# Kernel tuning notes

Measured on AMD Instinct MI355X. Metric: run time of the kernel, lower is better.

Reference implementation:

```python
import jax, jax.numpy as jnp
import numpy as np

B, L, DIM = 2, 2048, 1024
N_HEADS = 16
HEAD = DIM // N_HEADS  # 64


def setup_inputs() -> dict:
    key = jax.random.key(0)
    ks = jax.random.split(key, 7)
    s = 1.0 / np.sqrt(DIM)
    return {
        "q": jax.random.normal(ks[0], (B, L, DIM), jnp.float32),
        "k": jax.random.normal(ks[1], (B, L, DIM), jnp.float32),
        "v": jax.random.normal(ks[2], (B, L, DIM), jnp.float32),
        "Wq": jax.random.normal(ks[3], (DIM, DIM), jnp.float32) * s,
        "Wk": jax.random.normal(ks[4], (DIM, DIM), jnp.float32) * s,
        "Wv": jax.random.normal(ks[5], (DIM, DIM), jnp.float32) * s,
        "Wo": jax.random.normal(ks[6], (DIM, DIM), jnp.float32) * s,
    }


def reference(q, k, v, Wq, Wk, Wv, Wo):
    b, l, dim = q.shape
    # nn.Linear(bias=False): x @ W.T
    qp = (q @ Wq.T).reshape(b, N_HEADS, l, HEAD)  # faithful: plain view, no transpose-split
    kp = (k @ Wk.T).reshape(b, N_HEADS, l, HEAD)
    vp = (v @ Wv.T).reshape(b, N_HEADS, l, HEAD)
    attn_score = jnp.einsum('bnid,bnjd->bnij', qp, kp) / jnp.sqrt(jnp.float32(HEAD))
    attn_weight = jax.nn.softmax(attn_score, axis=3)  # dropout is identity at eval
    x = jnp.einsum('bnij,bnjd->bnid', attn_weight, vp)
    x = jnp.transpose(x, (0, 2, 1, 3)).reshape(b, l, dim)  # 'b n i d -> b i (n d)'
    return x @ Wo.T
```

## Files before the change

kernel.cpp:

```cpp
#include <hip/hip_runtime.h>
#include <hip/hip_bf16.h>

typedef __attribute__((ext_vector_type(8))) short short8;
typedef __attribute__((ext_vector_type(4))) float f32x4;
typedef __attribute__((ext_vector_type(2))) unsigned int u32x2;
typedef __attribute__((ext_vector_type(4))) unsigned int u32x4;

#define B_    2
#define L_    2048
#define DIM_  1024
#define NH_   16
#define HEAD_ 64
#define M_    4096
#define SZ_   4194304
#define WSZ_  1048576
#define SCL   0.18033688011112043f
#define MOFF  (72.0f * SCL)

#if __has_builtin(__builtin_amdgcn_exp2f)
#define EXP2(x) __builtin_amdgcn_exp2f(x)
#else
#define EXP2(x) exp2f(x)
#endif

#define BARRIER() asm volatile("s_barrier" ::: "memory")
#define VMW8()    asm volatile("s_waitcnt vmcnt(8)" ::: "memory")
#define VMW4()    asm volatile("s_waitcnt vmcnt(4)" ::: "memory")
#define VMW2()    asm volatile("s_waitcnt vmcnt(2)" ::: "memory")
#define VMW0()    asm volatile("s_waitcnt vmcnt(0)" ::: "memory")
#define SCHEDB()  __builtin_amdgcn_sched_barrier(0)

template<int N> struct IC { static constexpr int value = N; };

__device__ __forceinline__ unsigned short f2bf(float f) {
  __hip_bfloat16 h = __float2bfloat16(f);
  return __builtin_bit_cast(unsigned short, h);
}
__device__ __forceinline__ unsigned int pk2(float a, float b) {
  return (unsigned int)f2bf(a) | ((unsigned int)f2bf(b) << 16);
}
__device__ __forceinline__ void gl_lds16(const void* g, void* l) {
  __builtin_amdgcn_global_load_lds(
      (const __attribute__((address_space(1))) unsigned int*)g,
      (__attribute__((address_space(3))) unsigned int*)l, 16, 0, 0);
}

__device__ __forceinline__ void cvt_w_body(const float* src, unsigned short* dst, int blk) {
  const int idx = blk * 2048 + threadIdx.x * 8;
  f32x4 a = *(const f32x4*)(src + idx);
  f32x4 b = *(const f32x4*)(src + idx + 4);
  u32x4 o;
  o[0] = pk2(a[0], a[1]); o[1] = pk2(a[2], a[3]);
  o[2] = pk2(b[0], b[1]); o[3] = pk2(b[2], b[3]);
  *(u32x4*)(dst + idx) = o;
}
__device__ __forceinline__ void cvt_a_body(const float* src, unsigned short* dst, int blk) {
  const size_t i = ((size_t)blk * 256 + threadIdx.x) * 16;
  f32x4 a0 = *(const f32x4*)(src + i);
  f32x4 a1 = *(const f32x4*)(src + i + 4);
  f32x4 a2 = *(const f32x4*)(src + i + 8);
  f32x4 a3 = *(const f32x4*)(src + i + 12);
  u32x4 o0, o1;
  o0[0] = pk2(a0[0], a0[1]); o0[1] = pk2(a0[2], a0[3]);
  o0[2] = pk2(a1[0], a1[1]); o0[3] = pk2(a1[2], a1[3]);
  o1[0] = pk2(a2[0], a2[1]); o1[1] = pk2(a2[2], a2[3]);
  o1[2] = pk2(a3[0], a3[1]); o1[3] = pk2(a3[2], a3[3]);
  *(u32x4*)(dst + i)     = o0;
  *(u32x4*)(dst + i + 8) = o1;
}

__global__ __launch_bounds__(256) void cvt_all(const float* __restrict__ q,
                                               const float* __restrict__ k,
                                               const float* __restrict__ v,
                                               const float* __restrict__ w0,
                                               const float* __restrict__ w1,
                                               const float* __restrict__ w2,
                                               const float* __restrict__ w3,
                                               unsigned short* __restrict__ acts,
                                               unsigned short* __restrict__ Wb) {
  const int bid = blockIdx.x;
  if (bid < 2048) {
    const int w = bid >> 9;
    const float* src = (w == 0) ? w0 : (w == 1) ? w1 : (w == 2) ? w2 : w3;
    cvt_w_body(src, Wb + (size_t)w * WSZ_, bid & 511);
  } else {
    const int a   = (bid - 2048) >> 10;
    const int blk = (bid - 2048) & 1023;
    const float* src = (a == 0) ? q : (a == 1) ? k : v;
    cvt_a_body(src, acts + (size_t)a * SZ_, blk);
  }
}
__global__ __launch_bounds__(256) void cvt_w4(const float* __restrict__ w0,
                                              const float* __restrict__ w1,
                                              const float* __restrict__ w2,
                                              const float* __restrict__ w3,
                                              unsigned short* __restrict__ Wb) {
  const int w = blockIdx.x >> 9;
  const float* src = (w == 0) ? w0 : (w == 1) ? w1 : (w == 2) ? w2 : w3;
  cvt_w_body(src, Wb + (size_t)w * WSZ_, blockIdx.x & 511);
}
__global__ __launch_bounds__(256) void cvt_one(const float* __restrict__ src,
                                               unsigned short* __restrict__ dst) {
  cvt_a_body(src, dst, blockIdx.x);
}

template<int FINAL>
__global__ __launch_bounds__(256) void gemm_k(const unsigned short* __restrict__ Abase,
                                              size_t astride,
                                              const unsigned short* __restrict__ Wball,
                                              void* __restrict__ c0,
                                              unsigned short* __restrict__ vt,
                                              int gbase) {
  constexpr int Kdim = 1024, Ndim = 1024;
  __shared__ unsigned short Alds[2][128 * 64];
  __shared__ unsigned short Blds[2][128 * 64];
  const int t   = threadIdx.x;
  const int g   = gbase + (blockIdx.x >> 8);
  const int lin = blockIdx.x & 255;
  const int swz = (lin & 7) * 32 + (lin >> 3);
  const int m0  = (swz >> 3) * 128;
  const int n0  = (swz & 7) * 128;
  const int lane = t & 63;
  const int wid  = t >> 6;
  const int lr = lane & 15, lg = lane >> 4;
  const int wm = (wid >> 1) * 64, wn = (wid & 1) * 64;
  const int srow0 = wid * 8 + (lane >> 3);
  const int sj    = lane & 7;

  f32x4 acc[4][4] = {};

  const unsigned short* alane = Abase + (size_t)g * astride +
      (size_t)(m0 + srow0) * Kdim + (sj ^ (srow0 & 7)) * 8;
  const unsigned short* wlane = Wball + (size_t)g * WSZ_ +
      (size_t)(n0 + srow0) * Kdim + (sj ^ (srow0 & 7)) * 8;

  auto stage = [&](auto bufc) {
    constexpr int BUF = decltype(bufc)::value;
#pragma unroll
    for (int s = 0; s < 4; ++s)
      gl_lds16(alane + s * (32 * Kdim), (char*)Alds[BUF] + s * 4096 + wid * 1024);
#pragma unroll
    for (int s = 0; s < 4; ++s)
      gl_lds16(wlane + s * (32 * Kdim), (char*)Blds[BUF] + s * 4096 + wid * 1024);
    alane += 64; wlane += 64;
  };
  auto compute = [&](auto bufc) {
    constexpr int BUF = decltype(bufc)::value;
#pragma unroll
    for (int ks = 0; ks < 2; ++ks) {
      short8 af[4], bfv[4];
#pragma unroll
      for (int i = 0; i < 4; ++i) {
        const int r = wm + i * 16 + lr;
        af[i] = *(const short8*)((const char*)Alds[BUF] + r * 128 + ((ks * 64 + lg * 16) ^ ((r & 7) << 4)));
      }
#pragma unroll
      for (int j = 0; j < 4; ++j) {
        const int r = wn + j * 16 + lr;
        bfv[j] = *(const short8*)((const char*)Blds[BUF] + r * 128 + ((ks * 64 + lg * 16) ^ ((r & 7) << 4)));
      }
      __builtin_amdgcn_s_setprio(1);
#pragma unroll
      for (int i = 0; i < 4; ++i)
#pragma unroll
        for (int j = 0; j < 4; ++j)
          acc[i][j] = __builtin_amdgcn_mfma_f32_16x16x32_bf16(af[i], bfv[j], acc[i][j], 0, 0, 0);
      __builtin_amdgcn_s_setprio(0);
    }
  };

  stage(IC<0>{});
#pragma unroll 1
  for (int it = 0; it < 8; ++it) {
    stage(IC<1>{});
    SCHEDB(); VMW8(); BARRIER(); SCHEDB();
    compute(IC<0>{});
    BARRIER();
    if (it < 7) {
      stage(IC<0>{});
      SCHEDB(); VMW8(); BARRIER(); SCHEDB();
    } else {
      SCHEDB(); VMW0(); BARRIER(); SCHEDB();
    }
    compute(IC<1>{});
    BARRIER();
  }

  const float oscale = (FINAL == 0 && g == 0) ? SCL : 1.0f;
#pragma unroll
  for (int i = 0; i < 4; ++i) {
#pragma unroll
    for (int j = 0; j < 4; ++j) {
      const int grow = m0 + wm + i * 16 + lg * 4;
      const int gcol = n0 + wn + j * 16 + lr;
      if (FINAL) {
#pragma unroll
        for (int r = 0; r < 4; ++r)
          ((float*)c0)[(size_t)(grow + r) * Ndim + gcol] = acc[i][j][r];
      } else if (g == 2) {
        const int bh_  = grow >> 7;
        const int lrow = grow & 127;
        const int ch   = lrow >> 2;
        const int dd   = gcol & 63;
        const int cc   = gcol >> 6;
        const int pos  = ((cc >> 1) & 1) * 32 + (cc >> 2) * 8 + (cc & 1) * 4;
        u32x2 pk;
        pk[0] = pk2(acc[i][j][0], acc[i][j][1]);
        pk[1] = pk2(acc[i][j][2], acc[i][j][3]);
        *(u32x2*)&vt[((size_t)((bh_ * 32 + ch) * 64 + dd)) * 64 + pos] = pk;
      } else {
        unsigned short* out = (unsigned short*)c0 + (size_t)g * SZ_;
#pragma unroll
        for (int r = 0; r < 4; ++r)
          out[(size_t)(grow + r) * Ndim + gcol] = f2bf(acc[i][j][r] * oscale);
      }
    }
  }
}

__global__ __launch_bounds__(512, 2) void attn_flash(const unsigned short* __restrict__ QKV,
                                                     const unsigned short* __restrict__ VTg,
                                                     unsigned short* __restrict__ Xout) {
  __shared__ unsigned short Klds[3][64 * 64];
  __shared__ unsigned short VTlds[3][64 * 64];

  const int t    = threadIdx.x;
  const int wv   = t >> 6;
  const int lane = t & 63;
  const int lr   = lane & 15;
  const int lg   = lane >> 4;
  const int id  = blockIdx.x;
  const int xcd = id & 7;
  const int seq = id >> 3;
  const int bh  = xcd * 4 + (seq >> 3);
  const int qt  = seq & 7;
  const int b   = bh >> 4;
  const int h   = bh & 15;
  const size_t base = (size_t)b * (L_ * DIM_) + (size_t)h * (L_ * HEAD_);
  const unsigned short* Qp = QKV + base;
  const int q0 = qt * 256;
  const int srow0 = wv * 8 + (lane >> 3);
  const int sj    = lane & 7;

  short8 qf[2][2];
#pragma unroll
  for (int u = 0; u < 2; ++u)
#pragma unroll
    for (int ks = 0; ks < 2; ++ks)
      qf[u][ks] = *(const short8*)&Qp[(size_t)(q0 + wv * 32 + u * 16 + lr) * 64 + ks * 32 + lg * 8];

  f32x4 oacc[2][4] = {};
  f32x4 lsv[2] = {};

  const unsigned short* klane = QKV + (size_t)SZ_ + base + (size_t)srow0 * 64 + (sj ^ (srow0 & 7)) * 8;
  const unsigned short* vlane = VTg + (size_t)bh * (HEAD_ * L_) + (size_t)srow0 * 64 + (sj ^ (srow0 & 7)) * 8;

  auto stage = [&](auto bufc) {
    constexpr int BUF = decltype(bufc)::value;
    gl_lds16(klane, (char*)Klds[BUF] + wv * 1024);
    gl_lds16(vlane, (char*)VTlds[BUF] + wv * 1024);
    klane += 4096; vlane += 4096;
  };
  auto chunk = [&](auto bufc) {
    constexpr int BUF = decltype(bufc)::value;
    f32x4 sacc[2][4];
#pragma unroll
    for (int u = 0; u < 2; ++u)
#pragma unroll
      for (int jf = 0; jf < 4; ++jf)
#pragma unroll
        for (int c = 0; c < 4; ++c) sacc[u][jf][c] = -MOFF;
    __builtin_amdgcn_s_setprio(1);
#pragma unroll
    for (int jf = 0; jf < 4; ++jf) {
      const int row = jf * 16 + lr;
#pragma unroll
      for (int ks = 0; ks < 2; ++ks) {
        short8 kf = *(const short8*)((const char*)Klds[BUF] + row * 128 + ((ks * 64 + lg * 16) ^ ((row & 7) << 4)));
#pragma unroll
        for (int u = 0; u < 2; ++u)
          sacc[u][jf] = __builtin_amdgcn_mfma_f32_16x16x32_bf16(kf, qf[u][ks], sacc[u][jf], 0, 0, 0);
      }
    }
    __builtin_amdgcn_s_setprio(0);
    short8 pa[2][2];
#pragma unroll
    for (int u = 0; u < 2; ++u) {
      f32x4 p[4];
#pragma unroll
      for (int jf = 0; jf < 4; ++jf)
#pragma unroll
        for (int c = 0; c < 4; ++c)
          p[jf][c] = EXP2(sacc[u][jf][c]);
      f32x4 t0, t1;
#pragma unroll
      for (int c = 0; c < 4; ++c) { t0[c] = p[0][c] + p[1][c]; t1[c] = p[2][c] + p[3][c]; }
#pragma unroll
      for (int c = 0; c < 4; ++c) lsv[u][c] += t0[c] + t1[c];
      u32x4 w0, w1;
      w0[0] = pk2(p[0][0], p[1][0]); w0[1] = pk2(p[2][0], p[3][0]);
      w0[2] = pk2(p[0][1], p[1][1]); w0[3] = pk2(p[2][1], p[3][1]);
      w1[0] = pk2(p[0][2], p[1][2]); w1[1] = pk2(p[2][2], p[3][2]);
      w1[2] = pk2(p[0][3], p[1][3]); w1[3] = pk2(p[2][3], p[3][3]);
      pa[u][0] = __builtin_bit_cast(short8, w0);
      pa[u][1] = __builtin_bit_cast(short8, w1);
    }
#pragma unroll
    for (int kk = 0; kk < 2; ++kk) {
      __builtin_amdgcn_s_setprio(1);
#pragma unroll
      for (int nf = 0; nf < 4; ++nf) {
        const int rv = nf * 16 + lr;
        short8 vf = *(const short8*)((const char*)VTlds[BUF] + rv * 128 + ((kk * 64 + lg * 16) ^ ((rv & 7) << 4)));
#pragma unroll
        for (int u = 0; u < 2; ++u)
          oacc[u][nf] = __builtin_amdgcn_mfma_f32_16x16x32_bf16(pa[u][kk], vf, oacc[u][nf], 0, 0, 0);
      }
      __builtin_amdgcn_s_setprio(0);
    }
  };

  stage(IC<0>{});
  stage(IC<1>{});
#pragma unroll 1
  for (int it = 0; it < 10; ++it) {
    stage(IC<2>{});
    SCHEDB(); VMW4(); BARRIER(); SCHEDB();
    chunk(IC<0>{});
    BARRIER();
    stage(IC<0>{});
    SCHEDB(); VMW4(); BARRIER(); SCHEDB();
    chunk(IC<1>{});
    BARRIER();
    stage(IC<1>{});
    SCHEDB(); VMW4(); BARRIER(); SCHEDB();
    chunk(IC<2>{});
    BARRIER();
  }
  SCHEDB(); VMW2(); BARRIER(); SCHEDB();
  chunk(IC<0>{});
  SCHEDB(); VMW0(); BARRIER(); SCHEDB();
  chunk(IC<1>{});

#pragma unroll
  for (int u = 0; u < 2; ++u) {
    float ls = (lsv[u][0] + lsv[u][1]) + (lsv[u][2] + lsv[u][3]);
    ls += __shfl_xor(ls, 16, 64);
    ls += __shfl_xor(ls, 32, 64);
#pragma unroll
    for (int nf = 0; nf < 4; ++nf)
#pragma unroll
      for (int c = 0; c < 4; ++c) {
        const float lq = __shfl(ls, lg * 4 + c, 64);
        const int row = q0 + wv * 32 + u * 16 + lg * 4 + c;
        Xout[(size_t)b * (L_ * DIM_) + (size_t)row * DIM_ + h * HEAD_ + nf * 16 + lr] =
            f2bf(oacc[u][nf][c] / lq);
      }
  }
}

extern "C" void kernel_launch(void* const* d_in, const int* in_sizes, int n_in,
                              void* d_out, int out_size, void* d_ws, size_t ws_size,
                              hipStream_t stream) {
  (void)in_sizes; (void)n_in; (void)out_size;
  const float* q  = (const float*)d_in[0];
  const float* k  = (const float*)d_in[1];
  const float* v  = (const float*)d_in[2];
  const float* Wq = (const float*)d_in[3];
  const float* Wk = (const float*)d_in[4];
  const float* Wv = (const float*)d_in[5];
  const float* Wo = (const float*)d_in[6];

  unsigned short* wsu = (unsigned short*)d_ws;
  const bool fused = ws_size >= (size_t)(6 * (size_t)SZ_ + 4 * (size_t)WSZ_) * 2;

  if (fused) {
    unsigned short* acts = wsu;
    unsigned short* Wb   = wsu + 3 * (size_t)SZ_;
    unsigned short* qk   = Wb + 4 * (size_t)WSZ_;
    unsigned short* vt   = qk + 2 * (size_t)SZ_;
    unsigned short* xout = acts;

    cvt_all<<<5120, 256, 0, stream>>>(q, k, v, Wq, Wk, Wv, Wo, acts, Wb);
    gemm_k<0><<<768, 256, 0, stream>>>(acts, (size_t)SZ_, Wb, qk, vt, 0);
    attn_flash<<<256, 512, 0, stream>>>(qk, vt, xout);
    gemm_k<1><<<256, 256, 0, stream>>>(xout, 0, Wb, d_out, nullptr, 3);
  } else {
    unsigned short* xab = wsu;
    unsigned short* Wb  = wsu + (size_t)SZ_;
    unsigned short* qk  = Wb + 4 * (size_t)WSZ_;
    unsigned short* vt  = qk + 2 * (size_t)SZ_;

    cvt_w4<<<2048, 256, 0, stream>>>(Wq, Wk, Wv, Wo, Wb);
    cvt_one<<<1024, 256, 0, stream>>>(q, xab);
    gemm_k<0><<<256, 256, 0, stream>>>(xab, 0, Wb, qk, vt, 0);
    cvt_one<<<1024, 256, 0, stream>>>(k, xab);
    gemm_k<0><<<256, 256, 0, stream>>>(xab, 0, Wb, qk, vt, 1);
    cvt_one<<<1024, 256, 0, stream>>>(v, xab);
    gemm_k<0><<<256, 256, 0, stream>>>(xab, 0, Wb, qk, vt, 2);
    attn_flash<<<256, 512, 0, stream>>>(qk, vt, xab);
    gemm_k<1><<<256, 256, 0, stream>>>(xab, 0, Wb, d_out, nullptr, 3);
  }
}
```

Before: 116.2 us.

## Halve attention query tile per block and double grid for occupancy

Each attention block now processes 128 query rows instead of 256, with each wave handling one 16-row fragment instead of two, and the grid doubles to 512 blocks. This cuts per-thread accumulator registers and lets two blocks run per CU for better latency hiding. In exchange, K/V tiles loaded into LDS are reused by fewer queries, doubling K/V global reads and barrier overhead per unit of compute.

```diff
diff --git a/kernel.cpp b/kernel.cpp
--- a/kernel.cpp
+++ b/kernel.cpp
@@ -232,25 +232,23 @@
   const int id  = blockIdx.x;
   const int xcd = id & 7;
   const int seq = id >> 3;
-  const int bh  = xcd * 4 + (seq >> 3);
-  const int qt  = seq & 7;
+  const int bh  = xcd * 4 + (seq >> 4);
+  const int qt  = seq & 15;
   const int b   = bh >> 4;
   const int h   = bh & 15;
   const size_t base = (size_t)b * (L_ * DIM_) + (size_t)h * (L_ * HEAD_);
   const unsigned short* Qp = QKV + base;
-  const int q0 = qt * 256;
+  const int q0 = qt * 128;
   const int srow0 = wv * 8 + (lane >> 3);
   const int sj    = lane & 7;
 
-  short8 qf[2][2];
-#pragma unroll
-  for (int u = 0; u < 2; ++u)
-#pragma unroll
-    for (int ks = 0; ks < 2; ++ks)
-      qf[u][ks] = *(const short8*)&Qp[(size_t)(q0 + wv * 32 + u * 16 + lr) * 64 + ks * 32 + lg * 8];
-
-  f32x4 oacc[2][4] = {};
-  f32x4 lsv[2] = {};
+  short8 qf[2];
+#pragma unroll
+  for (int ks = 0; ks < 2; ++ks)
+    qf[ks] = *(const short8*)&Qp[(size_t)(q0 + wv * 16 + lr) * 64 + ks * 32 + lg * 8];
+
+  f32x4 oacc[4] = {};
+  f32x4 lsv = {};
 
   const unsigned short* klane = QKV + (size_t)SZ_ + base + (size_t)srow0 * 64 + (sj ^ (srow0 & 7)) * 8;
   const unsigned short* vlane = VTg + (size_t)bh * (HEAD_ * L_) + (size_t)srow0 * 64 + (sj ^ (srow0 & 7)) * 8;
@@ -263,13 +261,11 @@
   };
   auto chunk = [&](auto bufc) {
     constexpr int BUF = decltype(bufc)::value;
-    f32x4 sacc[2][4];
-#pragma unroll
-    for (int u = 0; u < 2; ++u)
-#pragma unroll
-      for (int jf = 0; jf < 4; ++jf)
-#pragma unroll
-        for (int c = 0; c < 4; ++c) sacc[u][jf][c] = -MOFF;
+    f32x4 sacc[4];
+#pragma unroll
+    for (int jf = 0; jf < 4; ++jf)
+#pragma unroll
+      for (int c = 0; c < 4; ++c) sacc[jf][c] = -MOFF;
     __builtin_amdgcn_s_setprio(1);
 #pragma unroll
     for (int jf = 0; jf < 4; ++jf) {
@@ -277,44 +273,37 @@
 #pragma unroll
       for (int ks = 0; ks < 2; ++ks) {
         short8 kf = *(const short8*)((const char*)Klds[BUF] + row * 128 + ((ks * 64 + lg * 16) ^ ((row & 7) << 4)));
-#pragma unroll
-        for (int u = 0; u < 2; ++u)
-          sacc[u][jf] = __builtin_amdgcn_mfma_f32_16x16x32_bf16(kf, qf[u][ks], sacc[u][jf], 0, 0, 0);
+        sacc[jf] = __builtin_amdgcn_mfma_f32_16x16x32_bf16(kf, qf[ks], sacc[jf], 0, 0, 0);
       }
     }
     __builtin_amdgcn_s_setprio(0);
-    short8 pa[2][2];
-#pragma unroll
-    for (int u = 0; u < 2; ++u) {
-      f32x4 p[4];
-#pragma unroll
-      for (int jf = 0; jf < 4; ++jf)
-#pragma unroll
-        for (int c = 0; c < 4; ++c)
-          p[jf][c] = EXP2(sacc[u][jf][c]);
-      f32x4 t0, t1;
-#pragma unroll
-      for (int c = 0; c < 4; ++c) { t0[c] = p[0][c] + p[1][c]; t1[c] = p[2][c] + p[3][c]; }
-#pragma unroll
-      for (int c = 0; c < 4; ++c) lsv[u][c] += t0[c] + t1[c];
-      u32x4 w0, w1;
-      w0[0] = pk2(p[0][0], p[1][0]); w0[1] = pk2(p[2][0], p[3][0]);
-      w0[2] = pk2(p[0][1], p[1][1]); w0[3] = pk2(p[2][1], p[3][1]);
-      w1[0] = pk2(p[0][2], p[1][2]); w1[1] = pk2(p[2][2], p[3][2]);
-      w1[2] = pk2(p[0][3], p[1][3]); w1[3] = pk2(p[2][3], p[3][3]);
-      pa[u][0] = __builtin_bit_cast(short8, w0);
-      pa[u][1] = __builtin_bit_cast(short8, w1);
-    }
+    f32x4 p[4];
+#pragma unroll
+    for (int jf = 0; jf < 4; ++jf)
+#pragma unroll
+      for (int c = 0; c < 4; ++c)
+        p[jf][c] = EXP2(sacc[jf][c]);
+    f32x4 t0, t1;
+#pragma unroll
+    for (int c = 0; c < 4; ++c) { t0[c] = p[0][c] + p[1][c]; t1[c] = p[2][c] + p[3][c]; }
+#pragma unroll
+    for (int c = 0; c < 4; ++c) lsv[c] += t0[c] + t1[c];
+    u32x4 w0, w1;
+    w0[0] = pk2(p[0][0], p[1][0]); w0[1] = pk2(p[2][0], p[3][0]);
+    w0[2] = pk2(p[0][1], p[1][1]); w0[3] = pk2(p[2][1], p[3][1]);
+    w1[0] = pk2(p[0][2], p[1][2]); w1[1] = pk2(p[2][2], p[3][2]);
+    w1[2] = pk2(p[0][3], p[1][3]); w1[3] = pk2(p[2][3], p[3][3]);
+    short8 pa0 = __builtin_bit_cast(short8, w0);
+    short8 pa1 = __builtin_bit_cast(short8, w1);
 #pragma unroll
     for (int kk = 0; kk < 2; ++kk) {
+      short8 pa = kk ? pa1 : pa0;
       __builtin_amdgcn_s_setprio(1);
 #pragma unroll
       for (int nf = 0; nf < 4; ++nf) {
         const int rv = nf * 16 + lr;
         short8 vf = *(const short8*)((const char*)VTlds[BUF] + rv * 128 + ((kk * 64 + lg * 16) ^ ((rv & 7) << 4)));
-#pragma unroll
-        for (int u = 0; u < 2; ++u)
-          oacc[u][nf] = __builtin_amdgcn_mfma_f32_16x16x32_bf16(pa[u][kk], vf, oacc[u][nf], 0, 0, 0);
+        oacc[nf] = __builtin_amdgcn_mfma_f32_16x16x32_bf16(pa, vf, oacc[nf], 0, 0, 0);
       }
       __builtin_amdgcn_s_setprio(0);
     }
@@ -342,21 +331,18 @@
   SCHEDB(); VMW0(); BARRIER(); SCHEDB();
   chunk(IC<1>{});
 
-#pragma unroll
-  for (int u = 0; u < 2; ++u) {
-    float ls = (lsv[u][0] + lsv[u][1]) + (lsv[u][2] + lsv[u][3]);
-    ls += __shfl_xor(ls, 16, 64);
-    ls += __shfl_xor(ls, 32, 64);
-#pragma unroll
-    for (int nf = 0; nf < 4; ++nf)
-#pragma unroll
-      for (int c = 0; c < 4; ++c) {
-        const float lq = __shfl(ls, lg * 4 + c, 64);
-        const int row = q0 + wv * 32 + u * 16 + lg * 4 + c;
-        Xout[(size_t)b * (L_ * DIM_) + (size_t)row * DIM_ + h * HEAD_ + nf * 16 + lr] =
-            f2bf(oacc[u][nf][c] / lq);
-      }
-  }
+  float ls = (lsv[0] + lsv[1]) + (lsv[2] + lsv[3]);
+  ls += __shfl_xor(ls, 16, 64);
+  ls += __shfl_xor(ls, 32, 64);
+#pragma unroll
+  for (int nf = 0; nf < 4; ++nf)
+#pragma unroll
+    for (int c = 0; c < 4; ++c) {
+      const float lq = __shfl(ls, lg * 4 + c, 64);
+      const int row = q0 + wv * 16 + lg * 4 + c;
+      Xout[(size_t)b * (L_ * DIM_) + (size_t)row * DIM_ + h * HEAD_ + nf * 16 + lr] =
+          f2bf(oacc[nf][c] / lq);
+    }
 }
 
 extern "C" void kernel_launch(void* const* d_in, const int* in_sizes, int n_in,
@@ -383,7 +369,7 @@
 
     cvt_all<<<5120, 256, 0, stream>>>(q, k, v, Wq, Wk, Wv, Wo, acts, Wb);
     gemm_k<0><<<768, 256, 0, stream>>>(acts, (size_t)SZ_, Wb, qk, vt, 0);
-    attn_flash<<<256, 512, 0, stream>>>(qk, vt, xout);
+    attn_flash<<<512, 512, 0, stream>>>(qk, vt, xout);
     gemm_k<1><<<256, 256, 0, stream>>>(xout, 0, Wb, d_out, nullptr, 3);
   } else {
     unsigned short* xab = wsu;
@@ -398,7 +384,7 @@
     gemm_k<0><<<256, 256, 0, stream>>>(xab, 0, Wb, qk, vt, 1);
     cvt_one<<<1024, 256, 0, stream>>>(v, xab);
     gemm_k<0><<<256, 256, 0, stream>>>(xab, 0, Wb, qk, vt, 2);
-    attn_flash<<<256, 512, 0, stream>>>(qk, vt, xab);
+    attn_flash<<<512, 512, 0, stream>>>(qk, vt, xab);
     gemm_k<1><<<256, 256, 0, stream>>>(xab, 0, Wb, d_out, nullptr, 3);
   }
 }
```

New measurement: 128.2 us. +10.4%, slower.
